# Optimization experiments

Hardware: AMD Instinct MI355X
Metric: run time of the kernel (lower is better)

The kernel has to match this reference:

```python
import jax, jax.numpy as jnp
import numpy as np

T = 4                      # number of time steps (args.T)
INITIAL_MEM = 0.5 * 1.0    # args.initial_mem * args.thresh


def real_threshes(raw_threshes):
    # softplus -> positive increments; cumsum -> ascending; flip -> descending
    inc = jax.nn.softplus(raw_threshes)
    return jnp.flip(jnp.cumsum(inc))


def _mlswat_core(x, th):
    # th is sorted descending. Exclusive selection in the torch loop picks the
    # FIRST (largest) threshold with x >= th_i, i.e. the largest th <= x.
    mask = x[..., None] >= th                      # [..., L]
    any_fire = mask.any(axis=-1)                   # [...]
    idx = jnp.argmax(mask, axis=-1)                # first True along L
    out = jnp.where(any_fire, th[idx], jnp.zeros((), x.dtype)).astype(x.dtype)
    return out, idx, any_fire


@jax.custom_vjp
def mlswat(x, th):
    out, _, _ = _mlswat_core(x, th)
    return out


def _mlswat_fwd(x, th):
    out, idx, any_fire = _mlswat_core(x, th)
    return out, (x, th, idx, any_fire)


def _mlswat_bwd(res, g):
    x, th, idx, any_fire = res
    L = th.shape[0]
    if L > 1:
        half_lower = (th[-2] - th[-1]) * 0.5
        half_upper = (th[0] - th[1]) * 0.5
    else:
        half_lower = th[0] * 0.5
        half_upper = half_lower
    lower = th[-1] - half_lower
    upper = th[0] + half_upper
    bmask = ((x >= lower) & (x <= upper)).astype(g.dtype)
    grad_in = g * bmask
    # grad wrt threshes: sum of g over elements whose exclusive slot is i
    g_sel = jnp.where(any_fire, g, jnp.zeros((), g.dtype))
    grad_th = jnp.zeros_like(th).at[idx.reshape(-1)].add(g_sel.reshape(-1))
    return grad_in, grad_th


mlswat.defvjp(_mlswat_fwd, _mlswat_bwd)


def setup_inputs() -> dict:
    key = jax.random.key(0)
    k1, k2, k3 = jax.random.split(key, 3)
    inputTensor = jax.random.normal(k1, (T, 16, 2048, 768), dtype=jnp.float32)
    raw_threshes = jax.random.normal(k2, (4,), dtype=jnp.float32)
    zero_point = jax.random.uniform(k3, (1,), dtype=jnp.float32)
    return {"inputTensor": inputTensor, "raw_threshes": raw_threshes,
            "zero_point": zero_point}


def reference(inputTensor, raw_threshes, zero_point):
    th = real_threshes(raw_threshes)
    aux = (zero_point / T)[0]                       # scalar auxiliary current
    v0 = jnp.full(inputTensor.shape[1:], INITIAL_MEM, dtype=inputTensor.dtype)

    def step(v, x_t):
        v = jax.lax.stop_gradient(v) + x_t + aux    # v.detach() + input + aux
        spikes = mlswat(v, th)
        v_next = v - jax.lax.stop_gradient(spikes)  # soft reset (detached)
        return v_next, spikes - aux

    _, out = jax.lax.scan(step, v0, inputTensor)    # out: [T, ...]
    return out
```

## Files before the change

### kernel.cpp

```cpp
#include <hip/hip_runtime.h>
#include <math.h>


static constexpr int TT = 4;
static constexpr int NSPAT = 16 * 2048 * 768;
static constexpr int N4 = NSPAT / 4;
static constexpr int HALF = N4 / 2;

typedef float f32x4 __attribute__((ext_vector_type(4)));

__global__ void compute_th_kernel(const float* __restrict__ raw,
                                  const float* __restrict__ zp,
                                  float* __restrict__ ws) {
    if (threadIdx.x == 0 && blockIdx.x == 0) {
        float inc[4];
#pragma unroll
        for (int i = 0; i < 4; ++i) {
            float x = raw[i];
            float a = -fabsf(x);
            float e = (float)exp((double)a);
            float l = (float)log1p((double)e);
            inc[i] = fmaxf(x, 0.0f) + l;
        }
        float c0 = inc[0];
        float c1 = c0 + inc[1];
        float c2 = c1 + inc[2];
        float c3 = c2 + inc[3];
        ws[0] = c3;
        ws[1] = c2;
        ws[2] = c1;
        ws[3] = c0;
        ws[4] = zp[0] / 4.0f;
    }
}

__device__ __forceinline__ float step1(float& v, float x, float aux,
                                       float th0, float th1, float th2,
                                       float th3) {
    v = (v + x) + aux;
    float s = (v >= th0) ? th0
            : (v >= th1) ? th1
            : (v >= th2) ? th2
            : (v >= th3) ? th3
            : 0.0f;
    v = v - s;
    return s - aux;
}

__device__ __forceinline__ f32x4 step4(f32x4& v, f32x4 xv, float aux,
                                       float t0, float t1, float t2, float t3) {
    f32x4 r;
#pragma unroll
    for (int k = 0; k < 4; ++k) {
        float vv = v[k];
        r[k] = step1(vv, xv[k], aux, t0, t1, t2, t3);
        v[k] = vv;
    }
    return r;
}

__global__ __launch_bounds__(256) void mlswat_fwd_kernel(
        const float* __restrict__ x,
        float* __restrict__ out,
        const float* __restrict__ ws) {
    const int i = blockIdx.x * blockDim.x + threadIdx.x;
    if (i >= HALF) return;
    const float th0 = ws[0], th1 = ws[1], th2 = ws[2], th3 = ws[3];
    const float aux = ws[4];

    const f32x4* __restrict__ xin = (const f32x4*)x;
    f32x4* __restrict__ o = (f32x4*)out;

    f32x4 va = {0.5f, 0.5f, 0.5f, 0.5f};
    f32x4 vb = va;
#pragma unroll
    for (int t = 0; t < TT; ++t) {
        const size_t base = (size_t)t * N4;
        f32x4 xa = __builtin_nontemporal_load(&xin[base + i]);
        f32x4 xb = __builtin_nontemporal_load(&xin[base + i + HALF]);
        f32x4 ra = step4(va, xa, aux, th0, th1, th2, th3);
        f32x4 rb = step4(vb, xb, aux, th0, th1, th2, th3);
        __builtin_nontemporal_store(ra, &o[base + i]);
        __builtin_nontemporal_store(rb, &o[base + i + HALF]);
    }
}

extern "C" void kernel_launch(void* const* d_in, const int* in_sizes, int n_in,
                              void* d_out, int out_size, void* d_ws, size_t ws_size,
                              hipStream_t stream) {
    const float* x   = (const float*)d_in[0];
    const float* raw = (const float*)d_in[1];
    const float* zp  = (const float*)d_in[2];
    float* out = (float*)d_out;
    float* ws  = (float*)d_ws;

    compute_th_kernel<<<1, 64, 0, stream>>>(raw, zp, ws);

    const int threads = 256;
    const int blocks = (HALF + threads - 1) / threads;
    mlswat_fwd_kernel<<<blocks, threads, 0, stream>>>(x, out, ws);
}
```

Before: 150.1 us.

## Fuse threshold computation into main kernel and hoist all timestep loads

Removes the separate single-thread threshold kernel; each block now computes the softplus/cumsum thresholds into shared memory behind a barrier, which saves one launch and a dependent kernel boundary. All eight vector loads per thread are issued up front before the recurrence so more memory requests are in flight. In exchange every block redoes the double-precision exp/log1p work on one thread, adds a __syncthreads, and holds more registers per thread.

```diff
diff --git a/kernel.cpp b/kernel.cpp
--- a/kernel.cpp
+++ b/kernel.cpp
@@ -8,31 +8,6 @@
 static constexpr int HALF = N4 / 2;
 
 typedef float f32x4 __attribute__((ext_vector_type(4)));
-
-__global__ void compute_th_kernel(const float* __restrict__ raw,
-                                  const float* __restrict__ zp,
-                                  float* __restrict__ ws) {
-    if (threadIdx.x == 0 && blockIdx.x == 0) {
-        float inc[4];
-#pragma unroll
-        for (int i = 0; i < 4; ++i) {
-            float x = raw[i];
-            float a = -fabsf(x);
-            float e = (float)exp((double)a);
-            float l = (float)log1p((double)e);
-            inc[i] = fmaxf(x, 0.0f) + l;
-        }
-        float c0 = inc[0];
-        float c1 = c0 + inc[1];
-        float c2 = c1 + inc[2];
-        float c3 = c2 + inc[3];
-        ws[0] = c3;
-        ws[1] = c2;
-        ws[2] = c1;
-        ws[3] = c0;
-        ws[4] = zp[0] / 4.0f;
-    }
-}
 
 __device__ __forceinline__ float step1(float& v, float x, float aux,
                                        float th0, float th1, float th2,
@@ -47,39 +22,63 @@
     return s - aux;
 }
 
-__device__ __forceinline__ f32x4 step4(f32x4& v, f32x4 xv, float aux,
-                                       float t0, float t1, float t2, float t3) {
-    f32x4 r;
+__global__ __launch_bounds__(256) void mlswat_fused_kernel(
+        const float* __restrict__ x,
+        const float* __restrict__ raw,
+        const float* __restrict__ zp,
+        float* __restrict__ out) {
+    __shared__ float sh[5];
+    if (threadIdx.x == 0) {
+        float inc[4];
 #pragma unroll
-    for (int k = 0; k < 4; ++k) {
-        float vv = v[k];
-        r[k] = step1(vv, xv[k], aux, t0, t1, t2, t3);
-        v[k] = vv;
+        for (int j = 0; j < 4; ++j) {
+            float r = raw[j];
+            float a = -fabsf(r);
+            float e = (float)exp((double)a);
+            float l = (float)log1p((double)e);
+            inc[j] = fmaxf(r, 0.0f) + l;
+        }
+        float c0 = inc[0];
+        float c1 = c0 + inc[1];
+        float c2 = c1 + inc[2];
+        float c3 = c2 + inc[3];
+        sh[0] = c3;
+        sh[1] = c2;
+        sh[2] = c1;
+        sh[3] = c0;
+        sh[4] = zp[0] / 4.0f;
     }
-    return r;
-}
+    __syncthreads();
+    const float th0 = sh[0], th1 = sh[1], th2 = sh[2], th3 = sh[3];
+    const float aux = sh[4];
 
-__global__ __launch_bounds__(256) void mlswat_fwd_kernel(
-        const float* __restrict__ x,
-        float* __restrict__ out,
-        const float* __restrict__ ws) {
     const int i = blockIdx.x * blockDim.x + threadIdx.x;
-    if (i >= HALF) return;
-    const float th0 = ws[0], th1 = ws[1], th2 = ws[2], th3 = ws[3];
-    const float aux = ws[4];
-
     const f32x4* __restrict__ xin = (const f32x4*)x;
     f32x4* __restrict__ o = (f32x4*)out;
+
+    f32x4 xa[TT], xb[TT];
+#pragma unroll
+    for (int t = 0; t < TT; ++t) {
+        const size_t base = (size_t)t * N4;
+        xa[t] = __builtin_nontemporal_load(&xin[base + i]);
+        xb[t] = __builtin_nontemporal_load(&xin[base + i + HALF]);
+    }
 
     f32x4 va = {0.5f, 0.5f, 0.5f, 0.5f};
     f32x4 vb = va;
 #pragma unroll
     for (int t = 0; t < TT; ++t) {
         const size_t base = (size_t)t * N4;
-        f32x4 xa = __builtin_nontemporal_load(&xin[base + i]);
-        f32x4 xb = __builtin_nontemporal_load(&xin[base + i + HALF]);
-        f32x4 ra = step4(va, xa, aux, th0, th1, th2, th3);
-        f32x4 rb = step4(vb, xb, aux, th0, th1, th2, th3);
+        f32x4 ra, rb;
+#pragma unroll
+        for (int k = 0; k < 4; ++k) {
+            float vv = va[k];
+            ra[k] = step1(vv, xa[t][k], aux, th0, th1, th2, th3);
+            va[k] = vv;
+            float vw = vb[k];
+            rb[k] = step1(vw, xb[t][k], aux, th0, th1, th2, th3);
+            vb[k] = vw;
+        }
         __builtin_nontemporal_store(ra, &o[base + i]);
         __builtin_nontemporal_store(rb, &o[base + i + HALF]);
     }
@@ -92,11 +91,8 @@
     const float* raw = (const float*)d_in[1];
     const float* zp  = (const float*)d_in[2];
     float* out = (float*)d_out;
-    float* ws  = (float*)d_ws;
-
-    compute_th_kernel<<<1, 64, 0, stream>>>(raw, zp, ws);
 
     const int threads = 256;
-    const int blocks = (HALF + threads - 1) / threads;
-    mlswat_fwd_kernel<<<blocks, threads, 0, stream>>>(x, out, ws);
+    const int blocks = HALF / threads;
+    mlswat_fused_kernel<<<blocks, threads, 0, stream>>>(x, raw, zp, out);
 }
```

New measurement: 150.9 us. Within noise of the previous version (+0.5%).
